# Kernel tuning notes

Measured on AMD Instinct MI355X. Metric: run time of the kernel, lower is better.

The kernel has to match this reference:

```python
import jax, jax.numpy as jnp
import numpy as np

C = 1024            # hidden_dim // compression_rate
IN_DIM = 1024
OUT_DIM = 1024
FFT_LEN = C // 2 + 1
CURV = 1e-4         # self.c
EPS = 1e-7
LN_EPS = 1e-5


def _mobius_scalar_mul(r, x, c):
    # r (x) x = tanh(r * atanh(sqrt(c)||x||)) * x / (sqrt(c)||x||)
    sqrt_c = jnp.sqrt(c)
    norm = jnp.maximum(jnp.linalg.norm(x, axis=-1, keepdims=True), EPS)
    scn = jnp.clip(sqrt_c * norm, EPS, 1.0 - 1e-5)
    return jnp.tanh(r * jnp.arctanh(scn)) * x / (sqrt_c * norm)


def _mobius_add(x, y, c):
    x2 = jnp.sum(x * x, axis=-1, keepdims=True)
    y2 = jnp.sum(y * y, axis=-1, keepdims=True)
    xy = jnp.sum(x * y, axis=-1, keepdims=True)
    num = (1.0 + 2.0 * c * xy + c * y2) * x + (1.0 - c * x2) * y
    den = 1.0 + 2.0 * c * xy + (c * c) * x2 * y2
    return num / jnp.maximum(den, EPS)


def _poincare_ball_layer(u, v, c, t):
    # geodesic-style interpolation: ((1-t) (x) u) (+) (t (x) v)
    return _mobius_add(_mobius_scalar_mul(1.0 - t, u, c),
                       _mobius_scalar_mul(t, v, c), c)


def setup_inputs() -> dict:
    key = jax.random.key(0)
    k_x, k_p, k_d = jax.random.split(key, 3)
    std = 0.02
    x = jax.random.normal(k_x, (4, 2048, IN_DIM), dtype=jnp.float32)
    proj_w = jax.random.normal(k_p, (C, IN_DIM), dtype=jnp.float32) * std
    freq_w = jnp.zeros((FFT_LEN,), dtype=jnp.float32)
    t = jnp.float32(0.3)
    ln_g = jnp.ones((C,), dtype=jnp.float32)
    ln_b = jnp.zeros((C,), dtype=jnp.float32)
    down_w = jax.random.normal(k_d, (OUT_DIM, C), dtype=jnp.float32) * std
    scale = jnp.float32(1.0)
    return {"x": x, "proj_w": proj_w, "ln_g": ln_g, "ln_b": ln_b,
            "freq_w": freq_w, "t": t, "down_w": down_w, "scale": scale}


def reference(x, proj_w, ln_g, ln_b, freq_w, t, down_w, scale):
    B, L, _ = x.shape
    # non-sep branch (hidden_dim > in_dim): silu(Linear(x))
    comp = jax.nn.silu(jnp.einsum('bli,ci->blc', x, proj_w))
    mu = jnp.mean(comp, axis=-1, keepdims=True)
    var = jnp.var(comp, axis=-1, keepdims=True)
    comp = (comp - mu) * jax.lax.rsqrt(var + LN_EPS) * ln_g + ln_b
    comp = comp.reshape(-1, C)                     # [B*L, C]
    Xf = jnp.fft.rfft(comp, axis=1)                # [B*L, C//2+1]
    w = jax.nn.softmax(freq_w)[None, :]
    flat = jnp.fft.irfft(Xf * w, n=C, axis=1)
    flat = jnp.nan_to_num(flat)
    shift = jnp.nan_to_num(t * flat)
    hyp = jnp.nan_to_num(_poincare_ball_layer(flat, shift, CURV, t))
    hyp = hyp.reshape(B, L, C)
    return jnp.einsum('blc,oc->blo', hyp, down_w) * scale
```

## Files before the change

### kernel.cpp

```cpp
#include <hip/hip_runtime.h>
#include <math.h>

typedef float f32x4 __attribute__((ext_vector_type(4)));
typedef __bf16 bf16x8 __attribute__((ext_vector_type(8)));

__device__ __forceinline__ unsigned short f2bf(float f) {
  unsigned u = __float_as_uint(f);
  unsigned r = (u + 0x7fffu + ((u >> 16) & 1u)) >> 16;
  return (unsigned short)r;
}
__device__ __forceinline__ float bf2f(unsigned short h) {
  return __uint_as_float(((unsigned)h) << 16);
}

__device__ __forceinline__ float blk_sum(float v, float* red, int tid) {
  #pragma unroll
  for (int o = 32; o; o >>= 1) v += __shfl_down(v, o);
  __syncthreads();
  if ((tid & 63) == 0) red[tid >> 6] = v;
  __syncthreads();
  return red[0] + red[1] + red[2] + red[3];
}

__global__ __launch_bounds__(256) void k_s(const float* __restrict__ fw,
                                           float* __restrict__ s,
                                           float* __restrict__ pw) {
  __shared__ float wsh[513];
  __shared__ float red[4];
  int tid = threadIdx.x;
  float m = -1e30f;
  for (int i = tid; i < 513; i += 256) m = fmaxf(m, fw[i]);
  #pragma unroll
  for (int o = 32; o; o >>= 1) m = fmaxf(m, __shfl_down(m, o));
  if ((tid & 63) == 0) red[tid >> 6] = m;
  __syncthreads();
  m = fmaxf(fmaxf(red[0], red[1]), fmaxf(red[2], red[3]));
  float sum = 0.f;
  for (int i = tid; i < 513; i += 256) {
    float e = expf(fw[i] - m);
    wsh[i] = e;
    sum += e;
  }
  sum = blk_sum(sum, red, tid);
  float inv = 1.f / sum;

  if (blockIdx.x == 0) {
    for (int i = tid; i < 513; i += 256) {
      float wn = wsh[i] * inv;
      float cf = (i == 0 || i == 512) ? 1.f : 2.f;
      pw[i] = cf * wn * wn * (1.f / 1024.f);
    }
  }

  int gid = blockIdx.x * 256 + tid;
  int d = gid >> 3;
  int chunk = gid & 7;
  float acc = 0.f;
  for (int f = 1 + chunk; f < 512; f += 8) {
    int p = (f * d) & 1023;
    acc += wsh[f] * __cosf(6.283185307179586f * (float)p * (1.f / 1024.f));
  }
  acc += __shfl_xor(acc, 1);
  acc += __shfl_xor(acc, 2);
  acc += __shfl_xor(acc, 4);
  if (chunk == 0) {
    float tot = wsh[0] + ((d & 1) ? -wsh[512] : wsh[512]) + 2.f * acc;
    s[d] = tot * inv * (1.f / 1024.f);
  }
}

__global__ __launch_bounds__(256) void k_prep(const float* __restrict__ x,
                                              const float* __restrict__ pw,
                                              const float* __restrict__ dw,
                                              const float* __restrict__ s,
                                              unsigned short* __restrict__ xb,
                                              unsigned short* __restrict__ pwb,
                                              unsigned short* __restrict__ dwb,
                                              unsigned short* __restrict__ Sb) {
  int b = blockIdx.x;
  int tid = threadIdx.x;
  if (b < 8192) {
    int i = b * 256 + tid;
    float4 v = ((const float4*)x)[i];
    ushort4 o;
    o.x = f2bf(v.x); o.y = f2bf(v.y); o.z = f2bf(v.z); o.w = f2bf(v.w);
    ((ushort4*)xb)[i] = o;
  } else if (b < 9216) {
    int i = (b - 8192) * 256 + tid;
    float4 v = ((const float4*)pw)[i];
    ushort4 o;
    o.x = f2bf(v.x); o.y = f2bf(v.y); o.z = f2bf(v.z); o.w = f2bf(v.w);
    ((ushort4*)pwb)[i] = o;
  } else if (b < 10240) {
    int i = (b - 9216) * 256 + tid;
    float4 v = ((const float4*)dw)[i];
    ushort4 o;
    o.x = f2bf(v.x); o.y = f2bf(v.y); o.z = f2bf(v.z); o.w = f2bf(v.w);
    ((ushort4*)dwb)[i] = o;
  } else {
    int idx = (b - 10240) * 256 + tid;
    int n = idx >> 8;
    int k0 = (idx & 255) * 4;
    ushort4 o;
    o.x = f2bf(s[(k0 + 0 - n) & 1023]);
    o.y = f2bf(s[(k0 + 1 - n) & 1023]);
    o.z = f2bf(s[(k0 + 2 - n) & 1023]);
    o.w = f2bf(s[(k0 + 3 - n) & 1023]);
    ((ushort4*)Sb)[idx] = o;
  }
}

__device__ __forceinline__ void gemm_body(const unsigned short* __restrict__ A,
                                          const unsigned short* __restrict__ B,
                                          int bm, int bn, int tid,
                                          char* AsB, char* BsB,
                                          f32x4 acc[4][4]) {
  const int lane = tid & 63;
  const int wave = tid >> 6;
  const int mhalf = (wave & 1) * 64;
  const int nhalf = (wave >> 1) * 64;
  const int ar = tid >> 3;
  const int ac = (((tid & 7) ^ (ar & 7))) * 8;
  const unsigned short* Abase = A + (size_t)(bm + ar) * 1024 + ac;
  const unsigned short* Bbase = B + (size_t)(bn + ar) * 1024 + ac;
  const int mrow = lane & 15;
  const int kq = lane >> 4;
  const int sw = mrow & 7;

  for (int kt = 0; kt < 16; ++kt) {
    const int k0 = kt * 64;
    #pragma unroll
    for (int r = 0; r < 4; ++r) {
      __builtin_amdgcn_global_load_lds(
          (const __attribute__((address_space(1))) void*)(Abase + (size_t)(r * 32) * 1024 + k0),
          (__attribute__((address_space(3))) void*)(AsB + r * 4096 + wave * 1024), 16, 0, 0);
      __builtin_amdgcn_global_load_lds(
          (const __attribute__((address_space(1))) void*)(Bbase + (size_t)(r * 32) * 1024 + k0),
          (__attribute__((address_space(3))) void*)(BsB + r * 4096 + wave * 1024), 16, 0, 0);
    }
    __syncthreads();
    #pragma unroll
    for (int kc = 0; kc < 2; ++kc) {
      const int chunk = (kc << 2) | kq;
      bf16x8 af[4], bfr[4];
      #pragma unroll
      for (int mt = 0; mt < 4; ++mt)
        af[mt] = *(const bf16x8*)(AsB + (mhalf + mt * 16 + mrow) * 128 + ((chunk ^ sw) << 4));
      #pragma unroll
      for (int nt = 0; nt < 4; ++nt)
        bfr[nt] = *(const bf16x8*)(BsB + (nhalf + nt * 16 + mrow) * 128 + ((chunk ^ sw) << 4));
      #pragma unroll
      for (int mt = 0; mt < 4; ++mt)
        #pragma unroll
        for (int nt = 0; nt < 4; ++nt)
          acc[mt][nt] = __builtin_amdgcn_mfma_f32_16x16x32_bf16(af[mt], bfr[nt], acc[mt][nt], 0, 0, 0);
    }
    __syncthreads();
  }
}

__global__ __launch_bounds__(256, 5) void k_gemm1w2(const unsigned short* __restrict__ xb,
                                                    const unsigned short* __restrict__ pwb,
                                                    const unsigned short* __restrict__ dwb,
                                                    const unsigned short* __restrict__ Sb,
                                                    unsigned short* __restrict__ comp,
                                                    unsigned short* __restrict__ W2) {
  __shared__ __align__(16) unsigned short As[128 * 64];
  __shared__ __align__(16) unsigned short Bs[64 * 64];
  const int tid = threadIdx.x;
  const int lane = tid & 63;
  const int wave = tid >> 6;
  const int mrow = lane & 15;
  const int kq = lane >> 4;
  const int sw = mrow & 7;
  char* AsB = (char*)As;
  char* BsB = (char*)Bs;

  if (blockIdx.x < 1024) {
    const int gid = blockIdx.x;
    const int xcd = gid & 7;
    const int j = gid >> 3;
    const int ntile = j & 15;
    const int bmIdx = xcd + 8 * (j >> 4);
    const int bm = bmIdx * 128;
    const int bn = ntile * 64;
    const int mhalf = (wave & 1) * 64;
    const int nhalf = (wave >> 1) * 32;
    f32x4 acc[4][2] = {};
    const int ar = tid >> 3;
    const int ac = (((tid & 7) ^ (ar & 7))) * 8;
    const unsigned short* Abase = xb + (size_t)(bm + ar) * 1024 + ac;
    const unsigned short* Bbase = pwb + (size_t)(bn + ar) * 1024 + ac;

    for (int kt = 0; kt < 16; ++kt) {
      const int k0 = kt * 64;
      #pragma unroll
      for (int r = 0; r < 4; ++r)
        __builtin_amdgcn_global_load_lds(
            (const __attribute__((address_space(1))) void*)(Abase + (size_t)(r * 32) * 1024 + k0),
            (__attribute__((address_space(3))) void*)(AsB + r * 4096 + wave * 1024), 16, 0, 0);
      #pragma unroll
      for (int r = 0; r < 2; ++r)
        __builtin_amdgcn_global_load_lds(
            (const __attribute__((address_space(1))) void*)(Bbase + (size_t)(r * 32) * 1024 + k0),
            (__attribute__((address_space(3))) void*)(BsB + r * 4096 + wave * 1024), 16, 0, 0);
      __syncthreads();
      #pragma unroll
      for (int kc = 0; kc < 2; ++kc) {
        const int chunk = (kc << 2) | kq;
        bf16x8 af[4], bfr[2];
        #pragma unroll
        for (int mt = 0; mt < 4; ++mt)
          af[mt] = *(const bf16x8*)(AsB + (mhalf + mt * 16 + mrow) * 128 + ((chunk ^ sw) << 4));
        #pragma unroll
        for (int nt = 0; nt < 2; ++nt)
          bfr[nt] = *(const bf16x8*)(BsB + (nhalf + nt * 16 + mrow) * 128 + ((chunk ^ sw) << 4));
        #pragma unroll
        for (int mt = 0; mt < 4; ++mt)
          #pragma unroll
          for (int nt = 0; nt < 2; ++nt)
            acc[mt][nt] = __builtin_amdgcn_mfma_f32_16x16x32_bf16(af[mt], bfr[nt], acc[mt][nt], 0, 0, 0);
      }
      __syncthreads();
    }

    const int col = bn + nhalf + (lane & 15);
    const int rbase = bm + mhalf + (lane >> 4) * 4;
    #pragma unroll
    for (int mt = 0; mt < 4; ++mt)
      #pragma unroll
      for (int r = 0; r < 4; ++r) {
        const int row = rbase + mt * 16 + r;
        #pragma unroll
        for (int nt = 0; nt < 2; ++nt) {
          float v = acc[mt][nt][r];
          comp[(size_t)row * 1024 + (col + nt * 16)] = f2bf(v / (1.f + expf(-v)));
        }
      }
    return;
  }

  const int wbid = blockIdx.x - 1024;
  const int bm = (wbid >> 4) * 64;
  const int bn = (wbid & 15) * 64;
  const int wm = wave & 1;
  const int wn = wave >> 1;
  f32x4 acc[2][2] = {};
  const int ar = tid >> 3;
  const int ac = (((tid & 7) ^ (ar & 7))) * 8;
  const unsigned short* Abase = dwb + (size_t)(bm + ar) * 1024 + ac;
  const unsigned short* Bbase = Sb + (size_t)(bn + ar) * 1024 + ac;
  for (int kt = 0; kt < 16; ++kt) {
    const int k0 = kt * 64;
    #pragma unroll
    for (int r = 0; r < 2; ++r) {
      __builtin_amdgcn_global_load_lds(
          (const __attribute__((address_space(1))) void*)(Abase + (size_t)(r * 32) * 1024 + k0),
          (__attribute__((address_space(3))) void*)(AsB + r * 4096 + wave * 1024), 16, 0, 0);
      __builtin_amdgcn_global_load_lds(
          (const __attribute__((address_space(1))) void*)(Bbase + (size_t)(r * 32) * 1024 + k0),
          (__attribute__((address_space(3))) void*)(BsB + r * 4096 + wave * 1024), 16, 0, 0);
    }
    __syncthreads();
    #pragma unroll
    for (int kc = 0; kc < 2; ++kc) {
      const int chunk = (kc << 2) | kq;
      bf16x8 af[2], bfr[2];
      #pragma unroll
      for (int mt = 0; mt < 2; ++mt)
        af[mt] = *(const bf16x8*)(AsB + (wm * 32 + mt * 16 + mrow) * 128 + ((chunk ^ sw) << 4));
      #pragma unroll
      for (int nt = 0; nt < 2; ++nt)
        bfr[nt] = *(const bf16x8*)(BsB + (wn * 32 + nt * 16 + mrow) * 128 + ((chunk ^ sw) << 4));
      #pragma unroll
      for (int mt = 0; mt < 2; ++mt)
        #pragma unroll
        for (int nt = 0; nt < 2; ++nt)
          acc[mt][nt] = __builtin_amdgcn_mfma_f32_16x16x32_bf16(af[mt], bfr[nt], acc[mt][nt], 0, 0, 0);
    }
    __syncthreads();
  }
  const int col = bn + wn * 32 + (lane & 15);
  const int rbase = bm + wm * 32 + (lane >> 4) * 4;
  #pragma unroll
  for (int mt = 0; mt < 2; ++mt)
    #pragma unroll
    for (int nt = 0; nt < 2; ++nt)
      #pragma unroll
      for (int r = 0; r < 4; ++r) {
        int row = rbase + mt * 16 + r;
        W2[(size_t)row * 1024 + (col + nt * 16)] = f2bf(acc[mt][nt][r]);
      }
}

__global__ __launch_bounds__(256) void k_ln(unsigned short* __restrict__ comp,
                                            const float* __restrict__ ln_g,
                                            const float* __restrict__ ln_b,
                                            const float* __restrict__ pw_par,
                                            float* __restrict__ u2) {
  __shared__ float red[4];
  __shared__ float re[512];
  __shared__ float im[512];
  const int tid = threadIdx.x;
  const size_t rowoff = (size_t)blockIdx.x * 1024;
  ushort4 cv = ((const ushort4*)(comp + rowoff))[tid];
  float x0 = bf2f(cv.x), x1 = bf2f(cv.y), x2 = bf2f(cv.z), x3 = bf2f(cv.w);
  float mu = blk_sum(x0 + x1 + x2 + x3, red, tid) * (1.f / 1024.f);
  float d0 = x0 - mu, d1 = x1 - mu, d2 = x2 - mu, d3 = x3 - mu;
  float var = blk_sum(d0 * d0 + d1 * d1 + d2 * d2 + d3 * d3, red, tid) * (1.f / 1024.f);
  float inv = rsqrtf(var + 1e-5f);
  float4 g = ((const float4*)ln_g)[tid];
  float4 b = ((const float4*)ln_b)[tid];
  float y0 = d0 * inv * g.x + b.x;
  float y1 = d1 * inv * g.y + b.y;
  float y2 = d2 * inv * g.z + b.z;
  float y3 = d3 * inv * g.w + b.w;
  ushort4 o;
  o.x = f2bf(y0); o.y = f2bf(y1); o.z = f2bf(y2); o.w = f2bf(y3);
  ((ushort4*)(comp + rowoff))[tid] = o;

  re[2 * tid] = y0;     im[2 * tid] = y1;
  re[2 * tid + 1] = y2; im[2 * tid + 1] = y3;
  __syncthreads();

  #pragma unroll
  for (int st = 8; st >= 0; --st) {
    const int half = 1 << st;
    const int pos = tid & (half - 1);
    const int i = ((tid >> st) << (st + 1)) | pos;
    const int j = i + half;
    float ur = re[i], ui = im[i];
    float vr = re[j], vi = im[j];
    float tr = ur - vr, ti = ui - vi;
    float c, sn;
    __sincosf(-3.14159265358979f * (float)pos / (float)half, &sn, &c);
    re[i] = ur + vr; im[i] = ui + vi;
    re[j] = tr * c - ti * sn;
    im[j] = tr * sn + ti * c;
    __syncthreads();
  }

  float partial = 0.f;
  #pragma unroll
  for (int q = 0; q < 2; ++q) {
    const int k = tid + q * 256;
    const int rk = __brev((unsigned)k) >> 23;
    const int mk = (512 - k) & 511;
    const int rmk = __brev((unsigned)mk) >> 23;
    float zr = re[rk], zi = im[rk];
    float mr = re[rmk], mi = im[rmk];
    float er = 0.5f * (zr + mr), ei = 0.5f * (zi - mi);
    float dr = zr - mr, di = zi + mi;
    float orr = 0.5f * di, oi = -0.5f * dr;
    float c, sn;
    __sincosf(-3.14159265358979f * (float)k * (1.f / 512.f), &sn, &c);
    float xr = er + orr * c - oi * sn;
    float xi = ei + orr * sn + oi * c;
    partial += pw_par[k] * (xr * xr + xi * xi);
  }
  if (tid == 0) {
    float x512 = re[0] - im[0];
    partial += pw_par[512] * x512 * x512;
  }
  float tot = blk_sum(partial, red, tid);
  if (tid == 0) u2[blockIdx.x] = tot;
}

__device__ __forceinline__ float gamma_from_u2(float U2, float tv) {
  const float sc = 0.01f;
  const float c = 1e-4f;
  float nrm = sqrtf(U2);
  float nu = fmaxf(nrm, 1e-7f);
  float su = fminf(fmaxf(sc * nu, 1e-7f), 1.f - 1e-5f);
  float Af = tanhf((1.f - tv) * atanhf(su)) / (sc * nu);
  float nvn = fmaxf(fabsf(tv) * nrm, 1e-7f);
  float svv = fminf(fmaxf(sc * nvn, 1e-7f), 1.f - 1e-5f);
  float Bf = tv * tanhf(tv * atanhf(svv)) / (sc * nvn);
  float x2s = Af * Af * U2, y2s = Bf * Bf * U2, xys = Af * Bf * U2;
  float numc = (1.f + 2.f * c * xys + c * y2s) * Af + (1.f - c * x2s) * Bf;
  float den = fmaxf(1.f + 2.f * c * xys + c * c * x2s * y2s, 1e-7f);
  return numc / den;
}

__global__ __launch_bounds__(256, 4) void k_gemm23(const unsigned short* __restrict__ comp,
                                                   const unsigned short* __restrict__ W2,
                                                   const float* __restrict__ u2,
                                                   const float* __restrict__ t_ptr,
                                                   const float* __restrict__ scale_ptr,
                                                   float* __restrict__ out) {
  __shared__ __align__(16) unsigned short As[128 * 64];
  __shared__ __align__(16) unsigned short Bs[128 * 64];
  __shared__ float gs[128];
  const int tid = threadIdx.x;
  const int lane = tid & 63;
  const int wave = tid >> 6;
  const int xcd = blockIdx.x & 7;
  const int j = blockIdx.x >> 3;
  const int ntile = j & 7;
  const int bmIdx = xcd + 8 * (j >> 3);
  const int bm = bmIdx * 128;
  const int bn = ntile * 128;

  if (tid < 128) gs[tid] = gamma_from_u2(u2[bm + tid], t_ptr[0]) * scale_ptr[0];

  f32x4 acc[4][4] = {};
  gemm_body(comp, W2, bm, bn, tid, (char*)As, (char*)Bs, acc);

  const int col = bn + (wave >> 1) * 64 + (lane & 15);
  const int rbase = bm + (wave & 1) * 64 + (lane >> 4) * 4;
  #pragma unroll
  for (int mt = 0; mt < 4; ++mt)
    #pragma unroll
    for (int r = 0; r < 4; ++r) {
      const int row = rbase + mt * 16 + r;
      const float gsc = gs[row - bm];
      #pragma unroll
      for (int nt = 0; nt < 4; ++nt)
        out[(size_t)row * 1024 + (col + nt * 16)] = acc[mt][nt][r] * gsc;
    }
}

extern "C" void kernel_launch(void* const* d_in, const int* in_sizes, int n_in,
                              void* d_out, int out_size, void* d_ws, size_t ws_size,
                              hipStream_t stream) {
  const float* x      = (const float*)d_in[0];
  const float* proj_w = (const float*)d_in[1];
  const float* ln_g   = (const float*)d_in[2];
  const float* ln_b   = (const float*)d_in[3];
  const float* freq_w = (const float*)d_in[4];
  const float* t_p    = (const float*)d_in[5];
  const float* down_w = (const float*)d_in[6];
  const float* scale  = (const float*)d_in[7];

  char* ws = (char*)d_ws;
  unsigned short* xb   = (unsigned short*)ws;
  unsigned short* pwb  = (unsigned short*)(ws + (16u << 20));
  unsigned short* dwb  = (unsigned short*)(ws + (18u << 20));
  unsigned short* comp = (unsigned short*)(ws + (20u << 20));
  unsigned short* Sb   = (unsigned short*)(ws + (36u << 20));
  unsigned short* W2   = (unsigned short*)(ws + (38u << 20));
  float* s_buf         = (float*)(ws + (40u << 20));
  float* pw_par        = (float*)(ws + (40u << 20) + 4096);
  float* u2            = (float*)(ws + (40u << 20) + 8192);

  k_s<<<32, 256, 0, stream>>>(freq_w, s_buf, pw_par);
  k_prep<<<11264, 256, 0, stream>>>(x, proj_w, down_w, s_buf, xb, pwb, dwb, Sb);
  k_gemm1w2<<<1280, 256, 0, stream>>>(xb, pwb, dwb, Sb, comp, W2);
  k_ln<<<8192, 256, 0, stream>>>(comp, ln_g, ln_b, pw_par, u2);
  k_gemm23<<<512, 256, 0, stream>>>(comp, W2, u2, t_p, scale, (float*)d_out);
}
```

Baseline: 190.8 us.

## Compute LayerNorm and FFT energy per wavefront with register shuffles

The LN+FFT kernel changes from one 256-thread block per row to one 64-lane wavefront per row. Each lane holds 16 elements in registers and runs a register/shuffle-based radix-2 FFT. This removes the shared-memory butterflies and the nine block-wide barriers per row, and uses wave-level shuffle reductions instead of block reductions. The cost is more registers per thread and more complex bit-reversed indexing, which could be wrong at the edges.

```diff
diff --git a/kernel.cpp b/kernel.cpp
--- a/kernel.cpp
+++ b/kernel.cpp
@@ -3,6 +3,7 @@
 
 typedef float f32x4 __attribute__((ext_vector_type(4)));
 typedef __bf16 bf16x8 __attribute__((ext_vector_type(8)));
+typedef unsigned short u16x8 __attribute__((ext_vector_type(8)));
 
 __device__ __forceinline__ unsigned short f2bf(float f) {
   unsigned u = __float_as_uint(f);
@@ -293,77 +294,134 @@
       }
 }
 
+#define BFLY(I, J, C, S)                                       \
+  {                                                            \
+    float tr_ = zr[J] * (C) - zi[J] * (S);                     \
+    float ti_ = zr[J] * (S) + zi[J] * (C);                     \
+    zr[J] = zr[I] - tr_; zi[J] = zi[I] - ti_;                  \
+    zr[I] += tr_;        zi[I] += ti_;                         \
+  }
+
 __global__ __launch_bounds__(256) void k_ln(unsigned short* __restrict__ comp,
                                             const float* __restrict__ ln_g,
                                             const float* __restrict__ ln_b,
                                             const float* __restrict__ pw_par,
                                             float* __restrict__ u2) {
-  __shared__ float red[4];
-  __shared__ float re[512];
-  __shared__ float im[512];
   const int tid = threadIdx.x;
-  const size_t rowoff = (size_t)blockIdx.x * 1024;
-  ushort4 cv = ((const ushort4*)(comp + rowoff))[tid];
-  float x0 = bf2f(cv.x), x1 = bf2f(cv.y), x2 = bf2f(cv.z), x3 = bf2f(cv.w);
-  float mu = blk_sum(x0 + x1 + x2 + x3, red, tid) * (1.f / 1024.f);
-  float d0 = x0 - mu, d1 = x1 - mu, d2 = x2 - mu, d3 = x3 - mu;
-  float var = blk_sum(d0 * d0 + d1 * d1 + d2 * d2 + d3 * d3, red, tid) * (1.f / 1024.f);
-  float inv = rsqrtf(var + 1e-5f);
-  float4 g = ((const float4*)ln_g)[tid];
-  float4 b = ((const float4*)ln_b)[tid];
-  float y0 = d0 * inv * g.x + b.x;
-  float y1 = d1 * inv * g.y + b.y;
-  float y2 = d2 * inv * g.z + b.z;
-  float y3 = d3 * inv * g.w + b.w;
-  ushort4 o;
-  o.x = f2bf(y0); o.y = f2bf(y1); o.z = f2bf(y2); o.w = f2bf(y3);
-  ((ushort4*)(comp + rowoff))[tid] = o;
-
-  re[2 * tid] = y0;     im[2 * tid] = y1;
-  re[2 * tid + 1] = y2; im[2 * tid + 1] = y3;
-  __syncthreads();
-
-  #pragma unroll
-  for (int st = 8; st >= 0; --st) {
-    const int half = 1 << st;
-    const int pos = tid & (half - 1);
-    const int i = ((tid >> st) << (st + 1)) | pos;
-    const int j = i + half;
-    float ur = re[i], ui = im[i];
-    float vr = re[j], vi = im[j];
-    float tr = ur - vr, ti = ui - vi;
+  const int lane = tid & 63;
+  const int wv = tid >> 6;
+  const int row = blockIdx.x * 4 + wv;
+  const size_t rowoff = (size_t)row * 1024;
+  const int bl = __brev((unsigned)lane) >> 26;
+  const int ybase = bl * 16;
+
+  const u16x8* src = (const u16x8*)(comp + rowoff + ybase);
+  u16x8 a0 = src[0], a1 = src[1];
+  float y[16];
+  #pragma unroll
+  for (int i = 0; i < 8; ++i) { y[i] = bf2f(a0[i]); y[8 + i] = bf2f(a1[i]); }
+
+  float s1 = 0.f;
+  #pragma unroll
+  for (int i = 0; i < 16; ++i) s1 += y[i];
+  #pragma unroll
+  for (int o = 32; o; o >>= 1) s1 += __shfl_xor(s1, o);
+  const float mu = s1 * (1.f / 1024.f);
+  float s2 = 0.f;
+  #pragma unroll
+  for (int i = 0; i < 16; ++i) { float d = y[i] - mu; s2 += d * d; }
+  #pragma unroll
+  for (int o = 32; o; o >>= 1) s2 += __shfl_xor(s2, o);
+  const float inv = rsqrtf(s2 * (1.f / 1024.f) + 1e-5f);
+
+  const float4* gp = (const float4*)(ln_g + ybase);
+  const float4* bp = (const float4*)(ln_b + ybase);
+  #pragma unroll
+  for (int q = 0; q < 4; ++q) {
+    float4 g = gp[q], b = bp[q];
+    y[4 * q + 0] = (y[4 * q + 0] - mu) * inv * g.x + b.x;
+    y[4 * q + 1] = (y[4 * q + 1] - mu) * inv * g.y + b.y;
+    y[4 * q + 2] = (y[4 * q + 2] - mu) * inv * g.z + b.z;
+    y[4 * q + 3] = (y[4 * q + 3] - mu) * inv * g.w + b.w;
+  }
+  u16x8 o0, o1;
+  #pragma unroll
+  for (int i = 0; i < 8; ++i) { o0[i] = f2bf(y[i]); o1[i] = f2bf(y[8 + i]); }
+  u16x8* dst = (u16x8*)(comp + rowoff + ybase);
+  dst[0] = o0; dst[1] = o1;
+
+  float zr[8], zi[8];
+  const int cmap[8] = {0, 4, 2, 6, 1, 5, 3, 7};
+  #pragma unroll
+  for (int r = 0; r < 8; ++r) { zr[r] = y[2 * cmap[r]]; zi[r] = y[2 * cmap[r] + 1]; }
+
+  #pragma unroll
+  for (int s = 1; s <= 6; ++s) {
+    const int half = 1 << (s - 1);
+    const int pos = lane & (half - 1);
     float c, sn;
     __sincosf(-3.14159265358979f * (float)pos / (float)half, &sn, &c);
-    re[i] = ur + vr; im[i] = ui + vi;
-    re[j] = tr * c - ti * sn;
-    im[j] = tr * sn + ti * c;
-    __syncthreads();
+    const bool hi = (lane & half) != 0;
+    #pragma unroll
+    for (int r = 0; r < 8; ++r) {
+      const float pr = __shfl_xor(zr[r], half);
+      const float pi = __shfl_xor(zi[r], half);
+      const float ur = hi ? pr : zr[r];
+      const float ui = hi ? pi : zi[r];
+      const float vr = hi ? zr[r] : pr;
+      const float vi = hi ? zi[r] : pi;
+      const float tr = vr * c - vi * sn;
+      const float ti = vr * sn + vi * c;
+      zr[r] = hi ? (ur - tr) : (ur + tr);
+      zi[r] = hi ? (ui - ti) : (ui + ti);
+    }
+  }
+  {
+    float c, sn;
+    __sincosf(-3.14159265358979f * (float)lane * (1.f / 64.f), &sn, &c);
+    BFLY(0, 1, c, sn); BFLY(2, 3, c, sn); BFLY(4, 5, c, sn); BFLY(6, 7, c, sn);
+  }
+  {
+    float ca, sa, cb, sb;
+    __sincosf(-3.14159265358979f * (float)lane * (1.f / 128.f), &sa, &ca);
+    __sincosf(-3.14159265358979f * (float)(64 + lane) * (1.f / 128.f), &sb, &cb);
+    BFLY(0, 2, ca, sa); BFLY(4, 6, ca, sa);
+    BFLY(1, 3, cb, sb); BFLY(5, 7, cb, sb);
+  }
+  {
+    float ca, sa, cb, sb, cc, sc, cd, sd;
+    __sincosf(-3.14159265358979f * (float)lane * (1.f / 256.f), &sa, &ca);
+    __sincosf(-3.14159265358979f * (float)(64 + lane) * (1.f / 256.f), &sb, &cb);
+    __sincosf(-3.14159265358979f * (float)(128 + lane) * (1.f / 256.f), &sc, &cc);
+    __sincosf(-3.14159265358979f * (float)(192 + lane) * (1.f / 256.f), &sd, &cd);
+    BFLY(0, 4, ca, sa); BFLY(1, 5, cb, sb); BFLY(2, 6, cc, sc); BFLY(3, 7, cd, sd);
   }
 
   float partial = 0.f;
-  #pragma unroll
-  for (int q = 0; q < 2; ++q) {
-    const int k = tid + q * 256;
-    const int rk = __brev((unsigned)k) >> 23;
-    const int mk = (512 - k) & 511;
-    const int rmk = __brev((unsigned)mk) >> 23;
-    float zr = re[rk], zi = im[rk];
-    float mr = re[rmk], mi = im[rmk];
-    float er = 0.5f * (zr + mr), ei = 0.5f * (zi - mi);
-    float dr = zr - mr, di = zi + mi;
-    float orr = 0.5f * di, oi = -0.5f * dr;
+  const int srcl = (64 - lane) & 63;
+  #pragma unroll
+  for (int r = 0; r < 8; ++r) {
+    const int k = r * 64 + lane;
+    float mr = __shfl(zr[7 - r], srcl);
+    float mi = __shfl(zi[7 - r], srcl);
+    if (lane == 0) { mr = zr[(8 - r) & 7]; mi = zi[(8 - r) & 7]; }
+    const float er = 0.5f * (zr[r] + mr);
+    const float ei = 0.5f * (zi[r] - mi);
+    const float orr = 0.5f * (zi[r] + mi);
+    const float oi = -0.5f * (zr[r] - mr);
     float c, sn;
     __sincosf(-3.14159265358979f * (float)k * (1.f / 512.f), &sn, &c);
-    float xr = er + orr * c - oi * sn;
-    float xi = ei + orr * sn + oi * c;
+    const float xr = er + orr * c - oi * sn;
+    const float xi = ei + orr * sn + oi * c;
     partial += pw_par[k] * (xr * xr + xi * xi);
   }
-  if (tid == 0) {
-    float x512 = re[0] - im[0];
+  if (lane == 0) {
+    const float x512 = zr[0] - zi[0];
     partial += pw_par[512] * x512 * x512;
   }
-  float tot = blk_sum(partial, red, tid);
-  if (tid == 0) u2[blockIdx.x] = tot;
+  #pragma unroll
+  for (int o = 32; o; o >>= 1) partial += __shfl_xor(partial, o);
+  if (lane == 0) u2[row] = partial;
 }
 
 __device__ __forceinline__ float gamma_from_u2(float U2, float tv) {
@@ -446,6 +504,6 @@
   k_s<<<32, 256, 0, stream>>>(freq_w, s_buf, pw_par);
   k_prep<<<11264, 256, 0, stream>>>(x, proj_w, down_w, s_buf, xb, pwb, dwb, Sb);
   k_gemm1w2<<<1280, 256, 0, stream>>>(xb, pwb, dwb, Sb, comp, W2);
-  k_ln<<<8192, 256, 0, stream>>>(comp, ln_g, ln_b, pw_par, u2);
+  k_ln<<<2048, 256, 0, stream>>>(comp, ln_g, ln_b, pw_par, u2);
   k_gemm23<<<512, 256, 0, stream>>>(comp, W2, u2, t_p, scale, (float*)d_out);
 }
```

After: 181.5 us. 4.9% less time.
